# Kernel optimization log

Measured on AMD Instinct MI355X. Metric: run time of the kernel, lower is better.

## Reference

```python
import jax, jax.numpy as jnp
import numpy as np

N = 50000
E = 1600000
H = 64          # hidden_dim
EIN = 8         # edges_in_d (7 edge feats + 1 distance)
NORM_FACTOR = 100.0
NORM_CONSTANT = 1.0


def setup_inputs() -> dict:
    key = jax.random.key(0)
    ks = jax.random.split(key, 9)
    h = jax.random.normal(ks[0], (N, H), dtype=jnp.float32)
    coord = jax.random.normal(ks[1], (N, 3), dtype=jnp.float32)
    edge_index = jax.random.randint(ks[2], (2, E), 0, N)
    edge_attr = jax.random.normal(ks[3], (E, EIN), dtype=jnp.float32)
    # coord_mlp params: Linear(2H+EIN,H) -> SiLU -> Linear(H,H) -> SiLU -> Linear(H,1,bias=False)
    din = 2 * H + EIN
    W1 = jax.random.normal(ks[4], (din, H), dtype=jnp.float32) / np.sqrt(din)
    b1 = jnp.zeros((H,), dtype=jnp.float32)
    W2 = jax.random.normal(ks[5], (H, H), dtype=jnp.float32) / np.sqrt(H)
    b2 = jnp.zeros((H,), dtype=jnp.float32)
    # final layer xavier_uniform with gain=0.001 -> very small weights
    W3 = jax.random.uniform(ks[6], (H, 1), dtype=jnp.float32, minval=-1.0, maxval=1.0) * (0.001 * np.sqrt(6.0 / (H + 1)))
    return {"h": h, "coord": coord, "edge_index": edge_index, "edge_attr": edge_attr,
            "W1": W1, "b1": b1, "W2": W2, "b2": b2, "W3": W3}


def reference(h, coord, edge_index, edge_attr, W1, b1, W2, b2, W3):
    row, col = edge_index[0], edge_index[1]
    # coord2diff (norm_constant=1)
    coord_diff = coord[row] - coord[col]                       # [E,3]
    radial = jnp.sum(coord_diff ** 2, axis=1, keepdims=True)   # [E,1]
    norm = jnp.sqrt(radial + 1e-8)
    coord_diff = coord_diff / (norm + NORM_CONSTANT)
    # gather + concat -> edge MLP (SiLU activations), tanh=False path
    inp = jnp.concatenate([h[row], h[col], edge_attr], axis=1)  # [E, 2H+EIN]
    x1 = jax.nn.silu(inp @ W1 + b1)
    x2 = jax.nn.silu(x1 @ W2 + b2)
    scal = x2 @ W3                                              # [E,1]
    trans = coord_diff * scal                                   # [E,3]
    # unsorted_segment_sum with 'sum' aggregation -> divide by normalization_factor
    agg = jax.ops.segment_sum(trans, row, num_segments=N) / NORM_FACTOR  # [N,3]
    return coord + agg
```

## Files before the change

kernel.cpp:

```cpp
#include <hip/hip_runtime.h>
#include <math.h>

#define HD   64
#define EIN  8
#define SAS  168
#define W2S  72
#define X1BS 72
#define NORM_INV 0.01f
#define NTH  256
#define NBLK 1536
#define NWAVES (NBLK * (NTH / 64))

typedef short bf16x8 __attribute__((ext_vector_type(8)));
typedef float f32x4  __attribute__((ext_vector_type(4)));
typedef float f4v    __attribute__((ext_vector_type(4)));

__device__ __forceinline__ unsigned short f2bf(float f) {
    union { float f; unsigned u; } v; v.f = f;
    unsigned r = v.u + 0x7FFFu + ((v.u >> 16) & 1u);
    return (unsigned short)(r >> 16);
}
__device__ __forceinline__ unsigned pk2(float a, float b) {
    return (unsigned)f2bf(a) | ((unsigned)f2bf(b) << 16);
}
__device__ __forceinline__ unsigned cvt_pk_bf16(float lo, float hi) {
    unsigned r;
    asm("v_cvt_pk_bf16_f32 %0, %1, %2" : "=v"(r) : "v"(lo), "v"(hi));
    return r;
}
__device__ __forceinline__ float silu_f(float x) {
    return x * __builtin_amdgcn_rcpf(1.0f + __expf(-x));
}
__device__ __forceinline__ void silu2(float x, float y, float& sx, float& sy) {
    float a = 1.0f + __expf(-x);
    float b = 1.0f + __expf(-y);
    float r = __builtin_amdgcn_rcpf(a * b);
    sx = x * (b * r);
    sy = y * (a * r);
}
__device__ __forceinline__ bf16x8 pack_f8(f4v a, f4v b) {
    union { bf16x8 v; uint4 u; } pk;
    pk.u.x = pk2(a.x, a.y); pk.u.y = pk2(a.z, a.w);
    pk.u.z = pk2(b.x, b.y); pk.u.w = pk2(b.z, b.w);
    return pk.v;
}

__global__ void prep_h_kernel(const float* __restrict__ h, unsigned char* __restrict__ hf8,
                              int nq, const float* __restrict__ coord,
                              float* __restrict__ out, int n3) {
    int i = blockIdx.x * blockDim.x + threadIdx.x;
    if (i < nq) {
        f4v v = reinterpret_cast<const f4v*>(h)[i];
        int p = __builtin_amdgcn_cvt_pk_fp8_f32(v.x, v.y, 0, false);
        p     = __builtin_amdgcn_cvt_pk_fp8_f32(v.z, v.w, p, true);
        reinterpret_cast<int*>(hf8)[i] = p;
    }
    if (i < n3) out[i] = coord[i];
}

__global__ void prep_out_kernel(const float* __restrict__ coord,
                                float* __restrict__ out, int n3) {
    int i = blockIdx.x * blockDim.x + threadIdx.x;
    if (i < n3) out[i] = coord[i];
}

template <bool HB>
__global__ __launch_bounds__(NTH, 5) void egnn_mfma_kernel(
    const float* __restrict__ h,
    const unsigned char* __restrict__ hf8,
    const float* __restrict__ coord,
    const int*   __restrict__ eidx,
    const float* __restrict__ eattr,
    const float* __restrict__ W1f,
    const float* __restrict__ W2f,
    const float* __restrict__ b1,
    const float* __restrict__ b2,
    const float* __restrict__ W3,
    float* __restrict__ out,
    int E_)
{
    constexpr int LDS_BYTES = HB ? 18688 : 40704;
    __shared__ __align__(16) char lds[LDS_BYTES];

    unsigned long*  sW1f8 = (unsigned long*)lds;
    unsigned short* sW1b  = (unsigned short*)(lds + 8192);
    unsigned long*  sW2f8 = (unsigned long*)(lds + 9216);
    unsigned char*  sX1b  = (unsigned char*)(lds + 13312);
    unsigned short* sW1   = (unsigned short*)lds;
    unsigned short* sW2   = (unsigned short*)(lds + 21504);
    unsigned short* sX1   = (unsigned short*)(lds + 30720);
    float*          sB1   = (float*)(lds + (HB ? 17920 : 39936));
    float*          sB2   = sB1 + 64;
    float*          sW3   = sB1 + 128;

    const int t = threadIdx.x;

    if (HB) {
        for (int f = t; f < 16 * 64; f += NTH) {
            int frag = f >> 6, ln = f & 63;
            int nt = frag >> 2, s = frag & 3;
            int mm = ln & 15, qq = ln >> 4;
            int n2 = nt * 16 + mm, kb = s * 32 + qq * 8;
            unsigned long v = 0;
#pragma unroll
            for (int j = 0; j < 8; j += 2) {
                float a = W1f[(kb + j) * 64 + n2] * 8.0f;
                float b = W1f[(kb + j + 1) * 64 + n2] * 8.0f;
                int p = __builtin_amdgcn_cvt_pk_fp8_f32(a, b, 0, false);
                v |= ((unsigned long)(unsigned)(p & 0xFFFF)) << (j * 8);
            }
            sW1f8[f] = v;
        }
        for (int i = t; i < 64 * 8; i += NTH) {
            int n2 = i >> 3, kk = i & 7;
            sW1b[i] = f2bf(W1f[(128 + kk) * 64 + n2]);
        }
        for (int f = t; f < 8 * 64; f += NTH) {
            int frag = f >> 6, ln = f & 63;
            int nt = frag >> 1, s = frag & 1;
            int mm = ln & 15, qq = ln >> 4;
            int n2 = nt * 16 + mm, kb = s * 32 + qq * 8;
            unsigned long v = 0;
#pragma unroll
            for (int j = 0; j < 8; j += 2) {
                float a = W2f[(kb + j) * 64 + n2] * 8.0f;
                float b = W2f[(kb + j + 1) * 64 + n2] * 8.0f;
                int p = __builtin_amdgcn_cvt_pk_fp8_f32(a, b, 0, false);
                v |= ((unsigned long)(unsigned)(p & 0xFFFF)) << (j * 8);
            }
            sW2f8[f] = v;
        }
    } else {
        for (int i = t; i < 136 * 64; i += NTH) {
            int k = i >> 6, n = i & 63;
            sW1[n * SAS + k] = f2bf(W1f[i]);
        }
        for (int i = t; i < 24 * 64; i += NTH) {
            int n = i / 24, k = 136 + (i - n * 24);
            sW1[n * SAS + k] = 0;
        }
        for (int i = t; i < 64 * 64; i += NTH) {
            int k = i >> 6, n = i & 63;
            sW2[n * W2S + k] = f2bf(W2f[i]);
        }
    }
    if (t < 64) sB1[t] = b1[t];
    else if (t < 128) sB2[t - 64] = b2[t - 64];
    else if (t < 192) sW3[t - 128] = W3[t - 128];
    __syncthreads();

    const int w = t >> 6, lane = t & 63;
    const int m = lane & 15, q = lane >> 4;

    unsigned char*  x1RowB = sX1b + (16 * w + m) * X1BS;
    unsigned short* x1Row  = sX1 + (16 * w + m) * W2S;

    const int ngroups = (E_ + 15) >> 4;
    for (int g = blockIdx.x * (NTH / 64) + w; g < ngroups; g += NWAVES) {
        int e = g * 16 + m;
        int ec = (e < E_) ? e : (E_ - 1);
        int row = __builtin_nontemporal_load(eidx + ec);
        int col = __builtin_nontemporal_load(eidx + (size_t)E_ + ec);

        float cr = 0.f, cc = 0.f;
        if (q < 3) { cr = coord[row * 3 + q]; cc = coord[col * 3 + q]; }

        bf16x8 bf4;
        {
            union { bf16x8 v; uint4 u; } pk;
            pk.u.x = 0; pk.u.y = 0; pk.u.z = 0; pk.u.w = 0;
            if (q == 0) {
                const f4v* ea = (const f4v*)(eattr + (size_t)ec * EIN);
                f4v a0 = __builtin_nontemporal_load(ea);
                f4v a1 = __builtin_nontemporal_load(ea + 1);
                pk.u.x = cvt_pk_bf16(a0.x, a0.y);
                pk.u.y = cvt_pk_bf16(a0.z, a0.w);
                pk.u.z = cvt_pk_bf16(a1.x, a1.y);
                pk.u.w = cvt_pk_bf16(a1.z, a1.w);
            }
            bf4 = pk.v;
        }

        f32x4 acc1[4] = {};

        if (HB) {
            const unsigned long* hr8 = (const unsigned long*)(hf8 + (size_t)row * HD);
            const unsigned long* hc8 = (const unsigned long*)(hf8 + (size_t)col * HD);
            long b0 = (long)hr8[q];
            long b1v = (long)hr8[4 + q];
            long b2v = (long)hc8[q];
            long b3v = (long)hc8[4 + q];
            __builtin_amdgcn_s_setprio(1);
#define L1F8(S, B)                                                            \
            _Pragma("unroll")                                                 \
            for (int nt = 0; nt < 4; ++nt) {                                  \
                long a8 = (long)sW1f8[((nt << 2) | (S)) * 64 + lane];         \
                acc1[nt] = __builtin_amdgcn_mfma_f32_16x16x32_fp8_fp8(a8, B, acc1[nt], 0, 0, 0); \
            }
            L1F8(0, b0)
            L1F8(1, b1v)
            L1F8(2, b2v)
            L1F8(3, b3v)
#undef L1F8
#pragma unroll
            for (int nt = 0; nt < 4; ++nt) {
                bf16x8 afb = *(const bf16x8*)(sW1b + (16 * nt + m) * 8);
                acc1[nt] = __builtin_amdgcn_mfma_f32_16x16x32_bf16(afb, bf4, acc1[nt], 0, 0, 0);
            }
            __builtin_amdgcn_s_setprio(0);
        } else {
            bf16x8 bf[5];
            const f4v* hr = (const f4v*)(h + (size_t)row * HD);
            const f4v* hc = (const f4v*)(h + (size_t)col * HD);
#pragma unroll
            for (int s = 0; s < 4; ++s) {
                const f4v* src = (s < 2) ? hr : hc;
                f4v a = src[(s & 1) * 8 + q * 2];
                f4v b = src[(s & 1) * 8 + q * 2 + 1];
                bf[s] = pack_f8(a, b);
            }
            bf[4] = bf4;
#pragma unroll
            for (int s = 0; s < 5; ++s) {
#pragma unroll
                for (int nt = 0; nt < 4; ++nt) {
                    bf16x8 afrag = *(const bf16x8*)(sW1 + (16 * nt + m) * SAS + s * 32 + q * 8);
                    acc1[nt] = __builtin_amdgcn_mfma_f32_16x16x32_bf16(afrag, bf[s], acc1[nt], 0, 0, 0);
                }
            }
        }

        const float sc = HB ? 0.125f : 1.0f;
#pragma unroll
        for (int nt = 0; nt < 4; ++nt) {
            float4 bb = *(const float4*)(&sB1[16 * nt + 4 * q]);
            float s0, s1, s2, s3;
            silu2(fmaf(acc1[nt][0], sc, bb.x), fmaf(acc1[nt][1], sc, bb.y), s0, s1);
            silu2(fmaf(acc1[nt][2], sc, bb.z), fmaf(acc1[nt][3], sc, bb.w), s2, s3);
            if (HB) {
                int p = __builtin_amdgcn_cvt_pk_fp8_f32(s0, s1, 0, false);
                p     = __builtin_amdgcn_cvt_pk_fp8_f32(s2, s3, p, true);
                *((unsigned*)(x1RowB + 16 * nt + 4 * q)) = (unsigned)p;
            } else {
                uint2 o;
                o.x = cvt_pk_bf16(s0, s1);
                o.y = cvt_pk_bf16(s2, s3);
                *((uint2*)(x1Row + 16 * nt + 4 * q)) = o;
            }
        }

        f32x4 acc2[4] = {};
        __builtin_amdgcn_s_setprio(1);
        if (HB) {
#pragma unroll
            for (int s = 0; s < 2; ++s) {
                long bfrag = *(const long*)(x1RowB + s * 32 + q * 8);
#pragma unroll
                for (int nt = 0; nt < 4; ++nt) {
                    long a8 = (long)sW2f8[((nt << 1) | s) * 64 + lane];
                    acc2[nt] = __builtin_amdgcn_mfma_f32_16x16x32_fp8_fp8(a8, bfrag, acc2[nt], 0, 0, 0);
                }
            }
        } else {
#pragma unroll
            for (int s = 0; s < 2; ++s) {
                bf16x8 bfrag = *(const bf16x8*)(x1Row + s * 32 + q * 8);
#pragma unroll
                for (int nt = 0; nt < 4; ++nt) {
                    bf16x8 afrag = *(const bf16x8*)(sW2 + (16 * nt + m) * W2S + s * 32 + q * 8);
                    acc2[nt] = __builtin_amdgcn_mfma_f32_16x16x32_bf16(afrag, bfrag, acc2[nt], 0, 0, 0);
                }
            }
        }
        __builtin_amdgcn_s_setprio(0);

        const float sc2 = HB ? 0.125f : 1.0f;
        float p = 0.f;
#pragma unroll
        for (int nt = 0; nt < 4; ++nt) {
            float4 b2v2 = *(const float4*)(&sB2[16 * nt + 4 * q]);
            float4 w3v  = *(const float4*)(&sW3[16 * nt + 4 * q]);
            float s0, s1, s2, s3;
            silu2(fmaf(acc2[nt][0], sc2, b2v2.x), fmaf(acc2[nt][1], sc2, b2v2.y), s0, s1);
            silu2(fmaf(acc2[nt][2], sc2, b2v2.z), fmaf(acc2[nt][3], sc2, b2v2.w), s2, s3);
            p = fmaf(s0, w3v.x, p);
            p = fmaf(s1, w3v.y, p);
            p = fmaf(s2, w3v.z, p);
            p = fmaf(s3, w3v.w, p);
        }
        p += __shfl_xor(p, 16);
        p += __shfl_xor(p, 32);

        float cd = cr - cc;
        float r2 = cd * cd;
        r2 += __shfl_xor(r2, 16);
        r2 += __shfl_xor(r2, 32);
        if (e < E_ && q < 3) {
            float inv = __builtin_amdgcn_rcpf(sqrtf(r2 + 1e-8f) + 1.0f);
            atomicAdd(&out[row * 3 + q], cd * (p * NORM_INV * inv));
        }
    }
}

extern "C" void kernel_launch(void* const* d_in, const int* in_sizes, int n_in,
                              void* d_out, int out_size, void* d_ws, size_t ws_size,
                              hipStream_t stream) {
    const float* h         = (const float*)d_in[0];
    const float* coord     = (const float*)d_in[1];
    const int*   eidx      = (const int*)  d_in[2];
    const float* edge_attr = (const float*)d_in[3];
    const float* W1        = (const float*)d_in[4];
    const float* b1        = (const float*)d_in[5];
    const float* W2        = (const float*)d_in[6];
    const float* b2        = (const float*)d_in[7];
    const float* W3        = (const float*)d_in[8];
    float* out = (float*)d_out;

    int E_ = in_sizes[2] / 2;
    int n3 = out_size;
    int nf = in_sizes[0];

    if (ws_size >= (size_t)nf) {
        unsigned char* hf8 = (unsigned char*)d_ws;
        int nq = nf / 4;
        int pgrid = (nq > n3 ? nq : n3);
        hipLaunchKernelGGL(prep_h_kernel, dim3((pgrid + 255) / 256), dim3(256), 0, stream,
                           h, hf8, nq, coord, out, n3);
        hipLaunchKernelGGL((egnn_mfma_kernel<true>), dim3(NBLK), dim3(NTH), 0, stream,
                           h, hf8, coord, eidx, edge_attr, W1, W2, b1, b2, W3, out, E_);
    } else {
        hipLaunchKernelGGL(prep_out_kernel, dim3((n3 + 255) / 256), dim3(256), 0, stream,
                           coord, out, n3);
        hipLaunchKernelGGL((egnn_mfma_kernel<false>), dim3(NBLK), dim3(NTH), 0, stream,
                           h, (const unsigned char*)nullptr, coord, eidx, edge_attr,
                           W1, W2, b1, b2, W3, out, E_);
    }
}
```

Measured before the change: 220.9 us.

## Software-pipeline edge index and fp8 feature gathers across contiguous per-wave chunks

Each wave now handles a contiguous chunk of 16-edge groups instead of a grid-strided range. In the fp8 path it prefetches the next group's h fragments and coords, plus the indices two groups ahead, while the current group's MFMAs run. Empty asm barriers stop the compiler from sinking those loads, so gather latency can overlap compute. The cost is extra live registers, which may lower occupancy, and contiguous chunking changes the memory locality pattern.

```diff
diff --git a/kernel.cpp b/kernel.cpp
--- a/kernel.cpp
+++ b/kernel.cpp
@@ -14,6 +14,8 @@
 typedef short bf16x8 __attribute__((ext_vector_type(8)));
 typedef float f32x4  __attribute__((ext_vector_type(4)));
 typedef float f4v    __attribute__((ext_vector_type(4)));
+
+#define PINV(x) asm volatile("" : "+v"(x))
 
 __device__ __forceinline__ unsigned short f2bf(float f) {
     union { float f; unsigned u; } v; v.f = f;
@@ -156,14 +158,54 @@
     unsigned short* x1Row  = sX1 + (16 * w + m) * W2S;
 
     const int ngroups = (E_ + 15) >> 4;
-    for (int g = blockIdx.x * (NTH / 64) + w; g < ngroups; g += NWAVES) {
+    const int wid = blockIdx.x * (NTH / 64) + w;
+    const int chunk = (ngroups + NWAVES - 1) / NWAVES;
+    const int gbeg = wid * chunk;
+    int gend = gbeg + chunk; if (gend > ngroups) gend = ngroups;
+    if (gbeg >= gend) return;
+
+#define IDXLD(G, R, C) do {                                             \
+    int e_ = (G) * 16 + m;                                              \
+    int ec_ = (e_ < E_) ? e_ : (E_ - 1);                                \
+    R = __builtin_nontemporal_load(eidx + ec_);                         \
+    C = __builtin_nontemporal_load(eidx + (size_t)E_ + ec_);            \
+} while (0)
+
+#define FRAGLD(R, C, B0, B1, B2, B3, CR, CC) do {                       \
+    const unsigned long* hr_ = (const unsigned long*)(hf8 + (size_t)(R) * HD); \
+    const unsigned long* hc_ = (const unsigned long*)(hf8 + (size_t)(C) * HD); \
+    B0 = (long)hr_[q]; B1 = (long)hr_[4 + q];                           \
+    B2 = (long)hc_[q]; B3 = (long)hc_[4 + q];                           \
+    CR = 0.f; CC = 0.f;                                                 \
+    if (q < 3) { CR = coord[(R) * 3 + q]; CC = coord[(C) * 3 + q]; }    \
+} while (0)
+
+    int  row_c = 0, col_c = 0;
+    long cb0 = 0, cb1 = 0, cb2 = 0, cb3 = 0;
+    float cr_c = 0.f, cc_c = 0.f;
+    int  row_n = 0, col_n = 0;
+
+    if (HB) {
+        IDXLD(gbeg, row_c, col_c);
+        FRAGLD(row_c, col_c, cb0, cb1, cb2, cb3, cr_c, cc_c);
+        IDXLD(gbeg + 1, row_n, col_n);
+    }
+
+    for (int g = gbeg; g < gend; ++g) {
         int e = g * 16 + m;
         int ec = (e < E_) ? e : (E_ - 1);
-        int row = __builtin_nontemporal_load(eidx + ec);
-        int col = __builtin_nontemporal_load(eidx + (size_t)E_ + ec);
-
-        float cr = 0.f, cc = 0.f;
-        if (q < 3) { cr = coord[row * 3 + q]; cc = coord[col * 3 + q]; }
+
+        long nb0 = 0, nb1 = 0, nb2 = 0, nb3 = 0;
+        float cr_n = 0.f, cc_n = 0.f;
+        int row_t = 0, col_t = 0;
+        if (HB) {
+            FRAGLD(row_n, col_n, nb0, nb1, nb2, nb3, cr_n, cc_n);
+            IDXLD(g + 2, row_t, col_t);
+        } else {
+            IDXLD(g, row_c, col_c);
+            cr_c = 0.f; cc_c = 0.f;
+            if (q < 3) { cr_c = coord[row_c * 3 + q]; cc_c = coord[col_c * 3 + q]; }
+        }
 
         bf16x8 bf4;
         {
@@ -184,12 +226,6 @@
         f32x4 acc1[4] = {};
 
         if (HB) {
-            const unsigned long* hr8 = (const unsigned long*)(hf8 + (size_t)row * HD);
-            const unsigned long* hc8 = (const unsigned long*)(hf8 + (size_t)col * HD);
-            long b0 = (long)hr8[q];
-            long b1v = (long)hr8[4 + q];
-            long b2v = (long)hc8[q];
-            long b3v = (long)hc8[4 + q];
             __builtin_amdgcn_s_setprio(1);
 #define L1F8(S, B)                                                            \
             _Pragma("unroll")                                                 \
@@ -197,10 +233,10 @@
                 long a8 = (long)sW1f8[((nt << 2) | (S)) * 64 + lane];         \
                 acc1[nt] = __builtin_amdgcn_mfma_f32_16x16x32_fp8_fp8(a8, B, acc1[nt], 0, 0, 0); \
             }
-            L1F8(0, b0)
-            L1F8(1, b1v)
-            L1F8(2, b2v)
-            L1F8(3, b3v)
+            L1F8(0, cb0)
+            L1F8(1, cb1)
+            L1F8(2, cb2)
+            L1F8(3, cb3)
 #undef L1F8
 #pragma unroll
             for (int nt = 0; nt < 4; ++nt) {
@@ -210,8 +246,8 @@
             __builtin_amdgcn_s_setprio(0);
         } else {
             bf16x8 bf[5];
-            const f4v* hr = (const f4v*)(h + (size_t)row * HD);
-            const f4v* hc = (const f4v*)(h + (size_t)col * HD);
+            const f4v* hr = (const f4v*)(h + (size_t)row_c * HD);
+            const f4v* hc = (const f4v*)(h + (size_t)col_c * HD);
 #pragma unroll
             for (int s = 0; s < 4; ++s) {
                 const f4v* src = (s < 2) ? hr : hc;
@@ -291,15 +327,27 @@
         p += __shfl_xor(p, 16);
         p += __shfl_xor(p, 32);
 
-        float cd = cr - cc;
+        float cd = cr_c - cc_c;
         float r2 = cd * cd;
         r2 += __shfl_xor(r2, 16);
         r2 += __shfl_xor(r2, 32);
         if (e < E_ && q < 3) {
             float inv = __builtin_amdgcn_rcpf(sqrtf(r2 + 1e-8f) + 1.0f);
-            atomicAdd(&out[row * 3 + q], cd * (p * NORM_INV * inv));
-        }
-    }
+            atomicAdd(&out[row_c * 3 + q], cd * (p * NORM_INV * inv));
+        }
+
+        if (HB) {
+            PINV(nb0); PINV(nb1); PINV(nb2); PINV(nb3);
+            PINV(cr_n); PINV(cc_n);
+            PINV(row_t); PINV(col_t);
+            cb0 = nb0; cb1 = nb1; cb2 = nb2; cb3 = nb3;
+            cr_c = cr_n; cc_c = cc_n;
+            row_c = row_n; col_c = col_n;
+            row_n = row_t; col_n = col_t;
+        }
+    }
+#undef IDXLD
+#undef FRAGLD
 }
 
 extern "C" void kernel_launch(void* const* d_in, const int* in_sizes, int n_in,
```

Measured after the change: 239.6 us. +8.5%, slower.

## Privatize atomic scatter into multiple output copies and reduce afterward

Applied to the files above, without the earlier changes.

Scatter-add atomics now target one of up to 8 zeroed workspace copies of the output, chosen by block index, instead of a single output array. A new reduce kernel sums coord plus all copies into the final output. The aim is to spread atomic contention across more addresses and cache lines. The cost is extra zeroing, an extra kernel launch and reduction traffic, and a larger atomic working set.

```diff
diff --git a/kernel.cpp b/kernel.cpp
--- a/kernel.cpp
+++ b/kernel.cpp
@@ -47,7 +47,8 @@
 
 __global__ void prep_h_kernel(const float* __restrict__ h, unsigned char* __restrict__ hf8,
                               int nq, const float* __restrict__ coord,
-                              float* __restrict__ out, int n3) {
+                              float* __restrict__ out, int n3,
+                              float* __restrict__ zbase, int zcount) {
     int i = blockIdx.x * blockDim.x + threadIdx.x;
     if (i < nq) {
         f4v v = reinterpret_cast<const f4v*>(h)[i];
@@ -56,12 +57,24 @@
         reinterpret_cast<int*>(hf8)[i] = p;
     }
     if (i < n3) out[i] = coord[i];
+    for (int j = i; j < zcount; j += gridDim.x * blockDim.x) zbase[j] = 0.f;
 }
 
 __global__ void prep_out_kernel(const float* __restrict__ coord,
                                 float* __restrict__ out, int n3) {
     int i = blockIdx.x * blockDim.x + threadIdx.x;
     if (i < n3) out[i] = coord[i];
+}
+
+__global__ void reduce_out_kernel(const float* __restrict__ coord,
+                                  const float* __restrict__ copies,
+                                  float* __restrict__ out, int n3, int nc) {
+    int i = blockIdx.x * blockDim.x + threadIdx.x;
+    if (i < n3) {
+        float s = coord[i];
+        for (int c = 0; c < nc; ++c) s += copies[(size_t)c * n3 + i];
+        out[i] = s;
+    }
 }
 
 template <bool HB>
@@ -76,7 +89,9 @@
     const float* __restrict__ b1,
     const float* __restrict__ b2,
     const float* __restrict__ W3,
-    float* __restrict__ out,
+    float* __restrict__ obase,
+    int ncmask,
+    int n3r,
     int E_)
 {
     constexpr int LDS_BYTES = HB ? 18688 : 40704;
@@ -151,6 +166,8 @@
 
     const int w = t >> 6, lane = t & 63;
     const int m = lane & 15, q = lane >> 4;
+
+    float* osink = obase + (size_t)(blockIdx.x & ncmask) * n3r;
 
     unsigned char*  x1RowB = sX1b + (16 * w + m) * X1BS;
     unsigned short* x1Row  = sX1 + (16 * w + m) * W2S;
@@ -297,7 +314,7 @@
         r2 += __shfl_xor(r2, 32);
         if (e < E_ && q < 3) {
             float inv = __builtin_amdgcn_rcpf(sqrtf(r2 + 1e-8f) + 1.0f);
-            atomicAdd(&out[row * 3 + q], cd * (p * NORM_INV * inv));
+            atomicAdd(&osink[row * 3 + q], cd * (p * NORM_INV * inv));
         }
     }
 }
@@ -320,19 +337,30 @@
     int n3 = out_size;
     int nf = in_sizes[0];
 
-    if (ws_size >= (size_t)nf) {
+    size_t hfbytes = (size_t)nf;
+    if (ws_size >= hfbytes) {
         unsigned char* hf8 = (unsigned char*)d_ws;
+        int ncopies = 1;
+        if (ws_size >= hfbytes + 32ull * (size_t)n3)      ncopies = 8;
+        else if (ws_size >= hfbytes + 16ull * (size_t)n3) ncopies = 4;
+        float* copies = (float*)((char*)d_ws + hfbytes);
+        int zcount = (ncopies > 1) ? ncopies * n3 : 0;
+
         int nq = nf / 4;
         int pgrid = (nq > n3 ? nq : n3);
         hipLaunchKernelGGL(prep_h_kernel, dim3((pgrid + 255) / 256), dim3(256), 0, stream,
-                           h, hf8, nq, coord, out, n3);
+                           h, hf8, nq, coord, out, n3, copies, zcount);
         hipLaunchKernelGGL((egnn_mfma_kernel<true>), dim3(NBLK), dim3(NTH), 0, stream,
-                           h, hf8, coord, eidx, edge_attr, W1, W2, b1, b2, W3, out, E_);
+                           h, hf8, coord, eidx, edge_attr, W1, W2, b1, b2, W3,
+                           (ncopies > 1 ? copies : out), ncopies - 1, n3, E_);
+        if (ncopies > 1)
+            hipLaunchKernelGGL(reduce_out_kernel, dim3((n3 + 255) / 256), dim3(256), 0, stream,
+                               coord, copies, out, n3, ncopies);
     } else {
         hipLaunchKernelGGL(prep_out_kernel, dim3((n3 + 255) / 256), dim3(256), 0, stream,
                            coord, out, n3);
         hipLaunchKernelGGL((egnn_mfma_kernel<false>), dim3(NBLK), dim3(NTH), 0, stream,
                            h, (const unsigned char*)nullptr, coord, eidx, edge_attr,
-                           W1, W2, b1, b2, W3, out, E_);
-    }
-}
+                           W1, W2, b1, b2, W3, out, 0, n3, E_);
+    }
+}
```

After: 229.3 us. 1.04x slower.
